# Performance work log

Hardware: AMD Instinct MI355X
Metric: run time of the kernel (lower is better)

## Reference

```python
import jax, jax.numpy as jnp
import numpy as np

B, T, D, H, L = 4096, 128, 21, 64, 32  # batch, seq_len, input_size(sensors), hidden, latent


def _lstm_layer(x, h0, c0, Wih, Whh, bih, bhh):
    """Single LSTM layer, PyTorch gate order (i,f,g,o).
    x: [B,T,Din], h0/c0: [B,H]. Returns (outputs [B,T,H], h_T [B,H])."""
    # Precompute input contribution for all timesteps (one big GEMM)
    xW = jnp.einsum('btd,gd->btg', x, Wih) + (bih + bhh)  # [B,T,4H]

    def step(carry, xw_t):
        h, c = carry
        gates = xw_t + h @ Whh.T  # [B,4H]
        i, f, g, o = jnp.split(gates, 4, axis=-1)
        i = jax.nn.sigmoid(i)
        f = jax.nn.sigmoid(f)
        g = jnp.tanh(g)
        o = jax.nn.sigmoid(o)
        c = f * c + i * g
        h = o * jnp.tanh(c)
        return (h, c), h

    (hT, cT), hs = jax.lax.scan(step, (h0, c0), jnp.swapaxes(xW, 0, 1))
    return jnp.swapaxes(hs, 0, 1), hT


def setup_inputs() -> dict:
    key = jax.random.key(0)
    ks = jax.random.split(key, 24)
    sc = 1.0 / np.sqrt(H)
    r = lambda k, shape, s: jax.random.normal(k, shape, dtype=jnp.float32) * s
    inp = {"x": r(ks[0], (B, T, D), 1.0)}
    # encoder + decoder LSTM params, 2 layers each (layer0 input dim D, layer1 input dim H)
    names = ["eWih0", "eWhh0", "ebih0", "ebhh0", "eWih1", "eWhh1", "ebih1", "ebhh1",
             "dWih0", "dWhh0", "dbih0", "dbhh0", "dWih1", "dWhh1", "dbih1", "dbhh1"]
    shapes = [(4 * H, D), (4 * H, H), (4 * H,), (4 * H,),
              (4 * H, H), (4 * H, H), (4 * H,), (4 * H,)] * 2
    for i, (n, sh) in enumerate(zip(names, shapes)):
        inp[n] = r(ks[1 + i], sh, sc)
    inp["tlW"] = r(ks[17], (L, H), sc)   # to_latent
    inp["tlb"] = r(ks[18], (L,), sc)
    inp["flW"] = r(ks[19], (H, L), sc)   # from_latent
    inp["flb"] = r(ks[20], (H,), sc)
    inp["outW"] = r(ks[21], (D, H), sc)  # output_layer
    inp["outb"] = r(ks[22], (D,), sc)
    return inp


def reference(x, eWih0, eWhh0, ebih0, ebhh0, eWih1, eWhh1, ebih1, ebhh1,
              dWih0, dWhh0, dbih0, dbhh0, dWih1, dWhh1, dbih1, dbhh1,
              tlW, tlb, flW, flb, outW, outb):
    z = jnp.zeros((x.shape[0], H), dtype=x.dtype)
    # --- encode (dropout inactive in eval) ---
    h1, _ = _lstm_layer(x, z, z, eWih0, eWhh0, ebih0, ebhh0)
    _, hT2 = _lstm_layer(h1, z, z, eWih1, eWhh1, ebih1, ebhh1)
    latent = hT2 @ tlW.T + tlb  # [B,L]
    # --- decode with teacher forcing on time-reversed input ---
    h0 = latent @ flW.T + flb   # [B,H], repeated across both layers
    xr = x[:, ::-1, :]
    d1, _ = _lstm_layer(xr, h0, z, dWih0, dWhh0, dbih0, dbhh0)
    d2, _ = _lstm_layer(d1, h0, z, dWih1, dWhh1, dbih1, dbhh1)
    rec = (jnp.einsum('bth,dh->btd', d2, outW) + outb)[:, ::-1, :]
    return rec, latent
```

## Files before the change

### kernel.cpp

```cpp
#include <hip/hip_runtime.h>

#define B_ 4096
#define T_ 128
#define DD_ 21
#define H_ 64
#define L_ 32
#define DP_ 32

typedef _Float16 f16;
typedef _Float16 f16x8 __attribute__((ext_vector_type(8)));
typedef _Float16 f16x4 __attribute__((ext_vector_type(4)));
typedef float f32x4 __attribute__((ext_vector_type(4)));

#if __has_builtin(__builtin_amdgcn_exp2f)
#define EXP2F(x) __builtin_amdgcn_exp2f(x)
#else
#define EXP2F(x) exp2f(x)
#endif
#if __has_builtin(__builtin_amdgcn_rcpf)
#define RCPF(x) __builtin_amdgcn_rcpf(x)
#else
#define RCPF(x) (1.0f / (x))
#endif

__device__ __forceinline__ float sigmoid_(float x) {
    return RCPF(1.0f + EXP2F(-1.4426950408889634f * x));
}
__device__ __forceinline__ float tanh_(float x) {
    return 1.0f - 2.0f * RCPF(1.0f + EXP2F(2.8853900817779268f * x));
}

#define MFMA16(A, Bf, C) __builtin_amdgcn_mfma_f32_16x16x32_f16((A), (Bf), (C), 0, 0, 0)

__device__ __forceinline__ void ring_read(const f16* ring, int slot, int l15, int lh,
                                          f16x8& a0, f16x8& a1) {
    const char* base = (const char*)(ring + slot * 1024);
    const int sw = (l15 & 7) << 4;
    a0 = *(const f16x8*)(base + l15 * 128 + ((lh * 16) ^ sw));
    a1 = *(const f16x8*)(base + l15 * 128 + ((64 + lh * 16) ^ sw));
}
__device__ __forceinline__ void ring_write(f16* ring, int slot, int w, int l15, int lh,
                                           const f16* hh) {
    char* base = (char*)(ring + slot * 1024);
    const int colb = (w * 16 + l15) * 2;
#pragma unroll
    for (int r = 0; r < 4; ++r) {
        const int row = lh * 4 + r;
        *(f16*)(base + row * 128 + (colb ^ ((row & 7) << 4))) = hh[r];
    }
}

__global__ __launch_bounds__(256)
void padx_k(const float* __restrict__ x, f16* __restrict__ xpad)
{
    const int idx = blockIdx.x * blockDim.x + threadIdx.x;
    const size_t bt = (size_t)(idx >> 3);
    const int k0 = (idx & 7) * 4;
    const float* src = x + bt * DD_;
    f16x4 v;
#pragma unroll
    for (int j = 0; j < 4; ++j) {
        const int k = k0 + j;
        v[j] = (k < DD_) ? (f16)src[k] : (f16)0.0f;
    }
    *(f16x4*)(xpad + bt * DP_ + k0) = v;
}

template<bool IS_DEC>
__global__ __launch_bounds__(512, 2)
void lstm_pair_k(const f16* __restrict__ xpad,
                 const float* __restrict__ Wih0, const float* __restrict__ Whh0,
                 const float* __restrict__ bih0, const float* __restrict__ bhh0,
                 const float* __restrict__ Wih1, const float* __restrict__ Whh1,
                 const float* __restrict__ bih1, const float* __restrict__ bhh1,
                 const float* __restrict__ h0p,
                 float* __restrict__ hT_out,
                 const float* __restrict__ outW, const float* __restrict__ outb,
                 float* __restrict__ rec_out)
{
    __shared__ f16x8 wlds0[4][8][64];
    __shared__ f16x8 xlds0[4][4][64];
    __shared__ f16x8 wlds1[4][8][64];
    __shared__ f16x8 xlds1[4][8][64];
    __shared__ __align__(16) f16 ring0[2 * 1024];
    __shared__ __align__(16) f16 ring1[2 * 1024];

    const int tid  = threadIdx.x;
    const int wv   = tid >> 6;
    const int grp  = wv >> 2;
    const int w    = wv & 3;
    const int lane = tid & 63;
    const int l15  = lane & 15;
    const int lh   = lane >> 4;
    const int rbase = blockIdx.x * 16;

    const float* Wih = grp ? Wih1 : Wih0;
    const float* Whh = grp ? Whh1 : Whh0;
    const float* bih = grp ? bih1 : bih0;
    const float* bhh = grp ? bhh1 : bhh0;

    f32x4 bias4[4];
#pragma unroll
    for (int q = 0; q < 4; ++q) {
        const int g = (w + 4 * q) * 16 + l15;
#pragma unroll
        for (int kt = 0; kt < 2; ++kt) {
            const float* p = Whh + g * H_ + kt * 32 + lh * 8;
            f16x8 v;
#pragma unroll
            for (int j = 0; j < 8; ++j) v[j] = (f16)p[j];
            if (grp) wlds1[w][q * 2 + kt][lane] = v;
            else     wlds0[w][q * 2 + kt][lane] = v;
        }
        if (grp) {
#pragma unroll
            for (int kt = 0; kt < 2; ++kt) {
                const float* p = Wih + g * H_ + kt * 32 + lh * 8;
                f16x8 v;
#pragma unroll
                for (int j = 0; j < 8; ++j) v[j] = (f16)p[j];
                xlds1[w][q * 2 + kt][lane] = v;
            }
        } else {
            const float* p = Wih + g * DD_;
            f16x8 v;
#pragma unroll
            for (int j = 0; j < 8; ++j) {
                const int k = lh * 8 + j;
                v[j] = (k < DD_) ? (f16)p[k] : (f16)0.0f;
            }
            xlds0[w][q][lane] = v;
        }
        const float bv = bih[g] + bhh[g];
        bias4[q] = (f32x4){bv, bv, bv, bv};
    }

    f16x8 bO[2];
    float obias = 0.0f;
    if (IS_DEC && grp == 1) {
        const int d = w * 16 + l15;
        const bool valid = (w < 2) && (d < DD_);
#pragma unroll
        for (int kt = 0; kt < 2; ++kt) {
            f16x8 v;
#pragma unroll
            for (int j = 0; j < 8; ++j)
                v[j] = valid ? (f16)outW[d * H_ + kt * 32 + lh * 8 + j] : (f16)0.0f;
            bO[kt] = v;
        }
        if (valid) obias = outb[d];
    }

    {
        f16* ring = (tid < 256) ? ring0 : ring1;
        const int i = tid & 255;
        const int row = i >> 4;
        const int cq = i & 15;
        f16x4 v;
#pragma unroll
        for (int j = 0; j < 4; ++j)
            v[j] = IS_DEC ? (f16)h0p[(size_t)(rbase + row) * H_ + cq * 4 + j] : (f16)0.0f;
        char* base = (char*)(ring + 1024);
        *(f16x4*)(base + row * 128 + ((cq * 8) ^ ((row & 7) << 4))) = v;
    }

    f32x4 c4 = {0.f, 0.f, 0.f, 0.f};

    auto xaddr = [&](int t) -> const f16* {
        const int trd = IS_DEC ? (T_ - 1 - t) : t;
        return xpad + ((size_t)(rbase + l15) * T_ + trd) * DP_ + lh * 8;
    };
    f16x8 xA, pf[2];
    if (grp == 0) {
        xA = *(const f16x8*)xaddr(0);
        pf[1] = *(const f16x8*)xaddr(1);
    }

    __syncthreads();

#pragma unroll 2
    for (int s = 0; s < 130; ++s) {
        if (grp == 0) {
            if (s < T_) {
                const int tf = (s + 2 < T_) ? s + 2 : T_ - 1;
                pf[s & 1] = *(const f16x8*)xaddr(tf);
                f16x8 hA0, hA1;
                ring_read(ring0, (s + 1) & 1, l15, lh, hA0, hA1);
                f32x4 acc[4];
#pragma unroll
                for (int q = 0; q < 4; ++q) {
                    f32x4 a = MFMA16(xA, xlds0[w][q][lane], bias4[q]);
                    a = MFMA16(hA0, wlds0[w][q * 2 + 0][lane], a);
                    a = MFMA16(hA1, wlds0[w][q * 2 + 1][lane], a);
                    acc[q] = a;
                }
                f16 hh[4];
#pragma unroll
                for (int r = 0; r < 4; ++r) {
                    const float iv = sigmoid_(acc[0][r]);
                    const float fv = sigmoid_(acc[1][r]);
                    const float gv = tanh_(acc[2][r]);
                    const float ov = sigmoid_(acc[3][r]);
                    const float cn = fv * c4[r] + iv * gv;
                    c4[r] = cn;
                    hh[r] = (f16)(ov * tanh_(cn));
                }
                ring_write(ring0, s & 1, w, l15, lh, hh);
                xA = pf[(s + 1) & 1];
            }
        } else {
            if (s >= 1) {
                f16x8 hA0, hA1;
                ring_read(ring1, s & 1, l15, lh, hA0, hA1);

                if (IS_DEC && s >= 2) {
                    if (w < 2) {
                        f32x4 ao = {obias, obias, obias, obias};
                        ao = MFMA16(hA0, bO[0], ao);
                        ao = MFMA16(hA1, bO[1], ao);
                        const int d = w * 16 + l15;
                        if (d < DD_) {
                            const int t = s - 2;
#pragma unroll
                            for (int r = 0; r < 4; ++r)
                                rec_out[((size_t)(rbase + lh * 4 + r) * T_ + (T_ - 1 - t)) * DD_ + d] = ao[r];
                        }
                    }
                }

                if (s <= T_) {
                    f16x8 xA0, xA1;
                    ring_read(ring0, (s + 1) & 1, l15, lh, xA0, xA1);
                    f32x4 acc[4];
#pragma unroll
                    for (int q = 0; q < 4; ++q) {
                        f32x4 a = MFMA16(xA0, xlds1[w][q * 2 + 0][lane], bias4[q]);
                        a = MFMA16(xA1, xlds1[w][q * 2 + 1][lane], a);
                        a = MFMA16(hA0, wlds1[w][q * 2 + 0][lane], a);
                        a = MFMA16(hA1, wlds1[w][q * 2 + 1][lane], a);
                        acc[q] = a;
                    }
                    f16 hh[4];
                    float hvf[4];
#pragma unroll
                    for (int r = 0; r < 4; ++r) {
                        const float iv = sigmoid_(acc[0][r]);
                        const float fv = sigmoid_(acc[1][r]);
                        const float gv = tanh_(acc[2][r]);
                        const float ov = sigmoid_(acc[3][r]);
                        const float cn = fv * c4[r] + iv * gv;
                        c4[r] = cn;
                        hvf[r] = ov * tanh_(cn);
                        hh[r] = (f16)hvf[r];
                    }
                    ring_write(ring1, (s + 1) & 1, w, l15, lh, hh);
                    if (!IS_DEC && s == T_) {
#pragma unroll
                        for (int r = 0; r < 4; ++r)
                            hT_out[(size_t)(rbase + lh * 4 + r) * H_ + w * 16 + l15] = hvf[r];
                    }
                }
            }
        }
        __syncthreads();
    }
}

__global__ __launch_bounds__(256)
void latent_k(const float* __restrict__ hT, const float* __restrict__ tlW,
              const float* __restrict__ tlb, const float* __restrict__ flW,
              const float* __restrict__ flb, float* __restrict__ lat_out,
              float* __restrict__ h0_out)
{
    __shared__ float lat[64][L_];
    const int tid = threadIdx.x;
    const int r = tid >> 2;
    const int rb = blockIdx.x * 64;

    float hr[H_];
    const float* hrow = hT + (size_t)(rb + r) * H_;
#pragma unroll
    for (int k = 0; k < H_; ++k) hr[k] = hrow[k];

    const int c8 = (tid & 3) * 8;
#pragma unroll
    for (int jj = 0; jj < 8; ++jj) {
        const int l = c8 + jj;
        float s = tlb[l];
        const float* wrow = tlW + l * H_;
#pragma unroll
        for (int k = 0; k < H_; ++k) s += hr[k] * wrow[k];
        lat[r][l] = s;
        lat_out[(size_t)(rb + r) * L_ + l] = s;
    }
    __syncthreads();

    float lr[L_];
#pragma unroll
    for (int k = 0; k < L_; ++k) lr[k] = lat[r][k];
    const int hc16 = (tid & 3) * 16;
#pragma unroll
    for (int jj = 0; jj < 16; ++jj) {
        const int hc = hc16 + jj;
        float s = flb[hc];
        const float* wrow = flW + hc * L_;
#pragma unroll
        for (int k = 0; k < L_; ++k) s += lr[k] * wrow[k];
        h0_out[(size_t)(rb + r) * H_ + hc] = s;
    }
}

extern "C" void kernel_launch(void* const* d_in, const int* in_sizes, int n_in,
                              void* d_out, int out_size, void* d_ws, size_t ws_size,
                              hipStream_t stream)
{
    const float* x     = (const float*)d_in[0];
    const float* eWih0 = (const float*)d_in[1];
    const float* eWhh0 = (const float*)d_in[2];
    const float* ebih0 = (const float*)d_in[3];
    const float* ebhh0 = (const float*)d_in[4];
    const float* eWih1 = (const float*)d_in[5];
    const float* eWhh1 = (const float*)d_in[6];
    const float* ebih1 = (const float*)d_in[7];
    const float* ebhh1 = (const float*)d_in[8];
    const float* dWih0 = (const float*)d_in[9];
    const float* dWhh0 = (const float*)d_in[10];
    const float* dbih0 = (const float*)d_in[11];
    const float* dbhh0 = (const float*)d_in[12];
    const float* dWih1 = (const float*)d_in[13];
    const float* dWhh1 = (const float*)d_in[14];
    const float* dbih1 = (const float*)d_in[15];
    const float* dbhh1 = (const float*)d_in[16];
    const float* tlW   = (const float*)d_in[17];
    const float* tlb   = (const float*)d_in[18];
    const float* flW   = (const float*)d_in[19];
    const float* flb   = (const float*)d_in[20];
    const float* outW  = (const float*)d_in[21];
    const float* outb  = (const float*)d_in[22];

    float* rec = (float*)d_out;
    float* lat = rec + (size_t)B_ * T_ * DD_;

    char* ws = (char*)d_ws;
    f16*   xpad = (f16*)ws;
    float* hT2  = (float*)(ws + (size_t)B_ * T_ * DP_ * 2);
    float* h0   = (float*)(ws + (size_t)B_ * T_ * DP_ * 2 + (size_t)B_ * H_ * 4);

    padx_k<<<dim3(B_ * T_ * 8 / 256), dim3(256), 0, stream>>>(x, xpad);
    lstm_pair_k<false><<<dim3(B_ / 16), dim3(512), 0, stream>>>(
        xpad, eWih0, eWhh0, ebih0, ebhh0, eWih1, eWhh1, ebih1, ebhh1,
        nullptr, hT2, nullptr, nullptr, nullptr);
    latent_k<<<dim3(B_ / 64), dim3(256), 0, stream>>>(hT2, tlW, tlb, flW, flb, lat, h0);
    lstm_pair_k<true><<<dim3(B_ / 16), dim3(512), 0, stream>>>(
        xpad, dWih0, dWhh0, dbih0, dbhh0, dWih1, dWhh1, dbih1, dbhh1,
        h0, nullptr, outW, outb, rec);
}
```

Measured before the change: 416.7 us.

## Keep LSTM weight fragments in registers and move output projection to layer-0 waves

Each wave now holds its Whh/Wih fp16 MFMA B-operand fragments in VGPRs instead of re-reading them from LDS every timestep, which removes per-step LDS traffic from the recurrence's critical path. The decoder output projection moves from layer-1 waves 0-1 to the less loaded layer-0 waves 2-3, balancing work between the two groups. The launch attribute is rewritten as an explicit waves-per-EU setting of two. The cost is higher register pressure, with a risk of spills, and one extra ring read per step on the layer-0 waves.

```diff
diff --git a/kernel.cpp b/kernel.cpp
--- a/kernel.cpp
+++ b/kernel.cpp
@@ -67,7 +67,8 @@
 }
 
 template<bool IS_DEC>
-__global__ __launch_bounds__(512, 2)
+__global__
+__attribute__((amdgpu_flat_work_group_size(512, 512), amdgpu_waves_per_eu(2, 2)))
 void lstm_pair_k(const f16* __restrict__ xpad,
                  const float* __restrict__ Wih0, const float* __restrict__ Whh0,
                  const float* __restrict__ bih0, const float* __restrict__ bhh0,
@@ -78,10 +79,6 @@
                  const float* __restrict__ outW, const float* __restrict__ outb,
                  float* __restrict__ rec_out)
 {
-    __shared__ f16x8 wlds0[4][8][64];
-    __shared__ f16x8 xlds0[4][4][64];
-    __shared__ f16x8 wlds1[4][8][64];
-    __shared__ f16x8 xlds1[4][8][64];
     __shared__ __align__(16) f16 ring0[2 * 1024];
     __shared__ __align__(16) f16 ring1[2 * 1024];
 
@@ -99,6 +96,8 @@
     const float* bih = grp ? bih1 : bih0;
     const float* bhh = grp ? bhh1 : bhh0;
 
+    f16x8 wR[8];
+    f16x8 xR[8];
     f32x4 bias4[4];
 #pragma unroll
     for (int q = 0; q < 4; ++q) {
@@ -109,8 +108,7 @@
             f16x8 v;
 #pragma unroll
             for (int j = 0; j < 8; ++j) v[j] = (f16)p[j];
-            if (grp) wlds1[w][q * 2 + kt][lane] = v;
-            else     wlds0[w][q * 2 + kt][lane] = v;
+            wR[q * 2 + kt] = v;
         }
         if (grp) {
 #pragma unroll
@@ -119,7 +117,7 @@
                 f16x8 v;
 #pragma unroll
                 for (int j = 0; j < 8; ++j) v[j] = (f16)p[j];
-                xlds1[w][q * 2 + kt][lane] = v;
+                xR[q * 2 + kt] = v;
             }
         } else {
             const float* p = Wih + g * DD_;
@@ -129,7 +127,7 @@
                 const int k = lh * 8 + j;
                 v[j] = (k < DD_) ? (f16)p[k] : (f16)0.0f;
             }
-            xlds0[w][q][lane] = v;
+            xR[q] = v;
         }
         const float bv = bih[g] + bhh[g];
         bias4[q] = (f32x4){bv, bv, bv, bv};
@@ -137,18 +135,18 @@
 
     f16x8 bO[2];
     float obias = 0.0f;
-    if (IS_DEC && grp == 1) {
-        const int d = w * 16 + l15;
-        const bool valid = (w < 2) && (d < DD_);
+    if (IS_DEC && grp == 0) {
+        const bool pvalid = (w >= 2) && ((w - 2) * 16 + l15 < DD_);
+        const int d = pvalid ? ((w - 2) * 16 + l15) : 0;
 #pragma unroll
         for (int kt = 0; kt < 2; ++kt) {
             f16x8 v;
 #pragma unroll
             for (int j = 0; j < 8; ++j)
-                v[j] = valid ? (f16)outW[d * H_ + kt * 32 + lh * 8 + j] : (f16)0.0f;
+                v[j] = pvalid ? (f16)outW[d * H_ + kt * 32 + lh * 8 + j] : (f16)0.0f;
             bO[kt] = v;
         }
-        if (valid) obias = outb[d];
+        if (pvalid) obias = outb[d];
     }
 
     {
@@ -189,9 +187,9 @@
                 f32x4 acc[4];
 #pragma unroll
                 for (int q = 0; q < 4; ++q) {
-                    f32x4 a = MFMA16(xA, xlds0[w][q][lane], bias4[q]);
-                    a = MFMA16(hA0, wlds0[w][q * 2 + 0][lane], a);
-                    a = MFMA16(hA1, wlds0[w][q * 2 + 1][lane], a);
+                    f32x4 a = MFMA16(xA, xR[q], bias4[q]);
+                    a = MFMA16(hA0, wR[q * 2 + 0], a);
+                    a = MFMA16(hA1, wR[q * 2 + 1], a);
                     acc[q] = a;
                 }
                 f16 hh[4];
@@ -208,57 +206,53 @@
                 ring_write(ring0, s & 1, w, l15, lh, hh);
                 xA = pf[(s + 1) & 1];
             }
+            if (IS_DEC && s >= 2 && w >= 2) {
+                f16x8 pA0, pA1;
+                ring_read(ring1, s & 1, l15, lh, pA0, pA1);
+                f32x4 ao = {obias, obias, obias, obias};
+                ao = MFMA16(pA0, bO[0], ao);
+                ao = MFMA16(pA1, bO[1], ao);
+                const int d = (w - 2) * 16 + l15;
+                if (d < DD_) {
+                    const int t = s - 2;
+#pragma unroll
+                    for (int r = 0; r < 4; ++r)
+                        rec_out[((size_t)(rbase + lh * 4 + r) * T_ + (T_ - 1 - t)) * DD_ + d] = ao[r];
+                }
+            }
         } else {
-            if (s >= 1) {
+            if (s >= 1 && s <= T_) {
                 f16x8 hA0, hA1;
                 ring_read(ring1, s & 1, l15, lh, hA0, hA1);
-
-                if (IS_DEC && s >= 2) {
-                    if (w < 2) {
-                        f32x4 ao = {obias, obias, obias, obias};
-                        ao = MFMA16(hA0, bO[0], ao);
-                        ao = MFMA16(hA1, bO[1], ao);
-                        const int d = w * 16 + l15;
-                        if (d < DD_) {
-                            const int t = s - 2;
-#pragma unroll
-                            for (int r = 0; r < 4; ++r)
-                                rec_out[((size_t)(rbase + lh * 4 + r) * T_ + (T_ - 1 - t)) * DD_ + d] = ao[r];
-                        }
-                    }
-                }
-
-                if (s <= T_) {
-                    f16x8 xA0, xA1;
-                    ring_read(ring0, (s + 1) & 1, l15, lh, xA0, xA1);
-                    f32x4 acc[4];
-#pragma unroll
-                    for (int q = 0; q < 4; ++q) {
-                        f32x4 a = MFMA16(xA0, xlds1[w][q * 2 + 0][lane], bias4[q]);
-                        a = MFMA16(xA1, xlds1[w][q * 2 + 1][lane], a);
-                        a = MFMA16(hA0, wlds1[w][q * 2 + 0][lane], a);
-                        a = MFMA16(hA1, wlds1[w][q * 2 + 1][lane], a);
-                        acc[q] = a;
-                    }
-                    f16 hh[4];
-                    float hvf[4];
-#pragma unroll
-                    for (int r = 0; r < 4; ++r) {
-                        const float iv = sigmoid_(acc[0][r]);
-                        const float fv = sigmoid_(acc[1][r]);
-                        const float gv = tanh_(acc[2][r]);
-                        const float ov = sigmoid_(acc[3][r]);
-                        const float cn = fv * c4[r] + iv * gv;
-                        c4[r] = cn;
-                        hvf[r] = ov * tanh_(cn);
-                        hh[r] = (f16)hvf[r];
-                    }
-                    ring_write(ring1, (s + 1) & 1, w, l15, lh, hh);
-                    if (!IS_DEC && s == T_) {
-#pragma unroll
-                        for (int r = 0; r < 4; ++r)
-                            hT_out[(size_t)(rbase + lh * 4 + r) * H_ + w * 16 + l15] = hvf[r];
-                    }
+                f16x8 xA0, xA1;
+                ring_read(ring0, (s + 1) & 1, l15, lh, xA0, xA1);
+                f32x4 acc[4];
+#pragma unroll
+                for (int q = 0; q < 4; ++q) {
+                    f32x4 a = MFMA16(xA0, xR[q * 2 + 0], bias4[q]);
+                    a = MFMA16(xA1, xR[q * 2 + 1], a);
+                    a = MFMA16(hA0, wR[q * 2 + 0], a);
+                    a = MFMA16(hA1, wR[q * 2 + 1], a);
+                    acc[q] = a;
+                }
+                f16 hh[4];
+                float hvf[4];
+#pragma unroll
+                for (int r = 0; r < 4; ++r) {
+                    const float iv = sigmoid_(acc[0][r]);
+                    const float fv = sigmoid_(acc[1][r]);
+                    const float gv = tanh_(acc[2][r]);
+                    const float ov = sigmoid_(acc[3][r]);
+                    const float cn = fv * c4[r] + iv * gv;
+                    c4[r] = cn;
+                    hvf[r] = ov * tanh_(cn);
+                    hh[r] = (f16)hvf[r];
+                }
+                ring_write(ring1, (s + 1) & 1, w, l15, lh, hh);
+                if (!IS_DEC && s == T_) {
+#pragma unroll
+                    for (int r = 0; r < 4; ++r)
+                        hT_out[(size_t)(rbase + lh * 4 + r) * H_ + w * 16 + l15] = hvf[r];
                 }
             }
         }
```

Measured after the change: 394.5 us. 5.3% less time.
